# Kernel tuning notes

Measured on AMD Instinct MI355X. Metric: run time of the kernel, lower is better.

The kernel has to match this reference:

```python
import jax, jax.numpy as jnp
import numpy as np

N_NODES = 50000
N_EDGES = 800000
IN_FEAT = 64
HIDDEN = 128
NUM_LAYERS = 3


def setup_inputs() -> dict:
    key = jax.random.key(0)
    ks = jax.random.split(key, 8)
    x = jax.random.normal(ks[0], (N_NODES, IN_FEAT), dtype=jnp.float32)
    edge_index = jax.random.randint(ks[1], (2, N_EDGES), 0, N_NODES, dtype=jnp.int64)
    s_in = 1.0 / np.sqrt(IN_FEAT)
    s_h = 1.0 / np.sqrt(HIDDEN)
    W_in = jax.random.uniform(ks[2], (IN_FEAT, HIDDEN), jnp.float32, -s_in, s_in)
    b_in = jax.random.uniform(ks[3], (HIDDEN,), jnp.float32, -s_in, s_in)
    W_self = jax.random.uniform(ks[4], (NUM_LAYERS, HIDDEN, HIDDEN), jnp.float32, -s_h, s_h)
    b_self = jax.random.uniform(ks[5], (NUM_LAYERS, HIDDEN), jnp.float32, -s_h, s_h)
    W_nbr = jax.random.uniform(ks[6], (NUM_LAYERS, HIDDEN, HIDDEN), jnp.float32, -s_h, s_h)
    return {"x": x, "edge_index": edge_index, "W_in": W_in, "b_in": b_in,
            "W_self": W_self, "b_self": b_self, "W_nbr": W_nbr}


def reference(x, edge_index, W_in, b_in, W_self, b_self, W_nbr):
    # input projection: h [N, HIDDEN]
    h = x @ W_in + b_in
    src = edge_index[0]
    dst = edge_index[1]
    n = h.shape[0]
    ones = jnp.ones((dst.shape[0], 1), dtype=h.dtype)
    # scatter-mean denominator is grad-constant; compute once
    cnt = jax.ops.segment_sum(ones, dst, num_segments=n)
    cnt = jnp.maximum(cnt, 1.0)
    for l in range(W_self.shape[0]):
        msg = h[src] @ W_nbr[l]                               # [E, HIDDEN]
        agg = jax.ops.segment_sum(msg, dst, num_segments=n) / cnt  # scatter-mean
        h = jax.nn.elu(h @ W_self[l] + b_self[l] + agg)
    return h
```

## Files before the change

### kernel.cpp

```cpp
#include <hip/hip_runtime.h>
#include <cstdint>

#define HIDDEN 128

typedef unsigned short u16;
using frag_t   = __attribute__((ext_vector_type(8))) short;
using f32x4_t  = __attribute__((ext_vector_type(4))) float;
using ushort8_t = __attribute__((ext_vector_type(8))) unsigned short;

__device__ __forceinline__ float bf2f(u16 u) {
    union { unsigned int i; float f; } c;
    c.i = ((unsigned int)u) << 16;
    return c.f;
}
__device__ __forceinline__ u16 f2bf(float f) {
    unsigned int u = __float_as_uint(f);
    unsigned int r = (u + 0x7fffu + ((u >> 16) & 1u)) >> 16;
    return (u16)r;
}


__global__ void k_hist_prep(const int* __restrict__ ei, int E, int* __restrict__ deg, int npr,
                            const float* __restrict__ x,
                            const float* __restrict__ W_in,
                            const float* __restrict__ W_self,
                            const float* __restrict__ W_nbr,
                            u16* __restrict__ xf,
                            u16* __restrict__ WtI_hi, u16* __restrict__ WtI_lo,
                            u16* __restrict__ WtS_hi, u16* __restrict__ WtS_lo,
                            u16* __restrict__ WtN_hi, u16* __restrict__ WtN_lo,
                            int L, int nxg) {
    {
        int r  = blockIdx.x & 7;
        int lo = r * npr, hi = lo + npr;
        int nb = gridDim.x >> 3;
        int bi = blockIdx.x >> 3;
        int tid = bi * blockDim.x + threadIdx.x;
        int stride = nb * blockDim.x;
        if ((E & 3) == 0) {
            const int4* d4 = (const int4*)(ei + E);
            int nch = E >> 2;
            for (int c = tid; c < nch; c += stride) {
                int4 d = d4[c];
                if (d.x >= lo && d.x < hi) atomicAdd(&deg[d.x], 1);
                if (d.y >= lo && d.y < hi) atomicAdd(&deg[d.y], 1);
                if (d.z >= lo && d.z < hi) atomicAdd(&deg[d.z], 1);
                if (d.w >= lo && d.w < hi) atomicAdd(&deg[d.w], 1);
            }
        } else {
            for (int e = tid; e < E; e += stride) {
                int d = ei[E + e];
                if (d >= lo && d < hi) atomicAdd(&deg[d], 1);
            }
        }
    }
    {
        int nIn = 64 * 128;
        int nSq = L * 128 * 128;
        int wtot = nIn + 2 * nSq;
        int total = wtot + nxg;
        int stride = gridDim.x * blockDim.x;
        for (int i = blockIdx.x * blockDim.x + threadIdx.x; i < total; i += stride) {
            if (i >= wtot) {
                int t = i - wtot;
                int row = t >> 3, c = t & 7;
                const float4* xs = (const float4*)(x + (size_t)row * 64 + c * 8);
                float4 v0 = xs[0], v1 = xs[1];
                ushort8_t o;
                o[0] = f2bf(v0.x); o[1] = f2bf(v0.y); o[2] = f2bf(v0.z); o[3] = f2bf(v0.w);
                o[4] = f2bf(v1.x); o[5] = f2bf(v1.y); o[6] = f2bf(v1.z); o[7] = f2bf(v1.w);
                int T = row >> 4, m = row & 15;
                int f = c >> 2, q = c & 3;
                *(ushort8_t*)&xf[((size_t)(T * 2 + f) * 64 + q * 16 + m) * 8] = o;
            } else {
                float v; u16* phi; u16* plo; int o;
                if (i < nIn) {
                    int n = i / 64, k = i % 64;
                    v = W_in[k * 128 + n]; phi = WtI_hi; plo = WtI_lo; o = n * 64 + k;
                } else if (i < nIn + nSq) {
                    int t = i - nIn;
                    int l = t / (128 * 128), r = t % (128 * 128);
                    int n = r / 128, k = r % 128;
                    v = W_self[l * 128 * 128 + k * 128 + n]; phi = WtS_hi; plo = WtS_lo;
                    o = l * 128 * 128 + n * 128 + k;
                } else {
                    int t = i - nIn - nSq;
                    int l = t / (128 * 128), r = t % (128 * 128);
                    int n = r / 128, k = r % 128;
                    v = W_nbr[l * 128 * 128 + k * 128 + n]; phi = WtN_hi; plo = WtN_lo;
                    o = l * 128 * 128 + n * 128 + k;
                }
                u16 hi = f2bf(v);
                phi[o] = hi;
                plo[o] = f2bf(v - bf2f(hi));
            }
        }
    }
}

__global__ void k_scan1(const int* __restrict__ deg, int* __restrict__ rowp,
                        int* __restrict__ bsums, int n) {
    __shared__ int sh[1024];
    int t = threadIdx.x;
    int base = blockIdx.x * 1024;
    int v = (base + t < n) ? deg[base + t] : 0;
    sh[t] = v;
    __syncthreads();
    for (int off = 1; off < 1024; off <<= 1) {
        int x = sh[t];
        int y = (t >= off) ? sh[t - off] : 0;
        __syncthreads();
        sh[t] = x + y;
        __syncthreads();
    }
    if (base + t < n) rowp[base + t + 1] = sh[t];
    if (t == 1023) bsums[blockIdx.x] = sh[1023];
}

__global__ void k_scan_tail(int* __restrict__ rowp, const int* __restrict__ bsums,
                            int* __restrict__ fillp, int n, int nb) {
    __shared__ int sh[1024];
    int t = threadIdx.x;
    int b = blockIdx.x;
    sh[t] = (t < nb) ? bsums[t] : 0;
    __syncthreads();
    for (int off = 1; off < 1024; off <<= 1) {
        int x = sh[t];
        int y = (t >= off) ? sh[t - off] : 0;
        __syncthreads();
        sh[t] = x + y;
        __syncthreads();
    }
    int boff = (b == 0) ? 0 : sh[b - 1];
    int base = b * 1024;
    if (base + t < n) {
        int v = rowp[base + t + 1] + boff;
        rowp[base + t + 1] = v;
        if (base + t + 1 < n) fillp[base + t + 1] = v;
    }
    if (b == 0 && t == 0) { rowp[0] = 0; fillp[0] = 0; }
}


__device__ __forceinline__ void dev_fill(const int* __restrict__ ei, int E,
                                         int* __restrict__ fillpos, int* __restrict__ colx,
                                         int npr, int bid, int nbF) {
    int r  = bid & 7;
    int lo = r * npr, hi = lo + npr;
    int nb = nbF >> 3;
    int bi = bid >> 3;
    int tid = bi * blockDim.x + threadIdx.x;
    int stride = nb * blockDim.x;
    if ((E & 3) == 0) {
        const int4* s4 = (const int4*)ei;
        const int4* d4 = (const int4*)(ei + E);
        int nch = E >> 2;
        for (int c = tid; c < nch; c += stride) {
            int4 d = d4[c];
            bool m0 = d.x >= lo && d.x < hi;
            bool m1 = d.y >= lo && d.y < hi;
            bool m2 = d.z >= lo && d.z < hi;
            bool m3 = d.w >= lo && d.w < hi;
            if (m0 | m1 | m2 | m3) {
                int4 s = s4[c];
                if (m0) colx[atomicAdd(&fillpos[d.x], 1)] = s.x;
                if (m1) colx[atomicAdd(&fillpos[d.y], 1)] = s.y;
                if (m2) colx[atomicAdd(&fillpos[d.z], 1)] = s.z;
                if (m3) colx[atomicAdd(&fillpos[d.w], 1)] = s.w;
            }
        }
    } else {
        for (int e = tid; e < E; e += stride) {
            int d = ei[E + e];
            if (d >= lo && d < hi) colx[atomicAdd(&fillpos[d], 1)] = ei[e];
        }
    }
}


__global__ __launch_bounds__(256, 4) void k_agg(
        const ushort8_t* __restrict__ hb8, const int* __restrict__ rowp,
        const int* __restrict__ colx, u16* __restrict__ Sf, int n) {
    int g = (blockIdx.x * blockDim.x + threadIdx.x) >> 4;
    int lane = threadIdx.x & 15;
    if (g >= n) return;
    int beg = rowp[g];
    int end = rowp[g + 1];
    float a0[8], a1[8];
#pragma unroll
    for (int j = 0; j < 8; ++j) { a0[j] = 0.f; a1[j] = 0.f; }
    int e = beg;
    for (; e + 15 < end; e += 16) {
        int s0 = colx[e],      s1 = colx[e + 1],  s2 = colx[e + 2],  s3 = colx[e + 3];
        int s4 = colx[e + 4],  s5 = colx[e + 5],  s6 = colx[e + 6],  s7 = colx[e + 7];
        int s8 = colx[e + 8],  s9 = colx[e + 9],  sa = colx[e + 10], sb = colx[e + 11];
        int sc = colx[e + 12], sd = colx[e + 13], se = colx[e + 14], sf = colx[e + 15];
        ushort8_t v0 = hb8[(size_t)s0 * 16 + lane];
        ushort8_t v1 = hb8[(size_t)s1 * 16 + lane];
        ushort8_t v2 = hb8[(size_t)s2 * 16 + lane];
        ushort8_t v3 = hb8[(size_t)s3 * 16 + lane];
        ushort8_t v4 = hb8[(size_t)s4 * 16 + lane];
        ushort8_t v5 = hb8[(size_t)s5 * 16 + lane];
        ushort8_t v6 = hb8[(size_t)s6 * 16 + lane];
        ushort8_t v7 = hb8[(size_t)s7 * 16 + lane];
        ushort8_t v8 = hb8[(size_t)s8 * 16 + lane];
        ushort8_t v9 = hb8[(size_t)s9 * 16 + lane];
        ushort8_t va = hb8[(size_t)sa * 16 + lane];
        ushort8_t vb = hb8[(size_t)sb * 16 + lane];
        ushort8_t vc = hb8[(size_t)sc * 16 + lane];
        ushort8_t vd = hb8[(size_t)sd * 16 + lane];
        ushort8_t ve = hb8[(size_t)se * 16 + lane];
        ushort8_t vf = hb8[(size_t)sf * 16 + lane];
#pragma unroll
        for (int j = 0; j < 8; ++j) {
            a0[j] += bf2f(v0[j]); a1[j] += bf2f(v1[j]);
            a0[j] += bf2f(v2[j]); a1[j] += bf2f(v3[j]);
            a0[j] += bf2f(v4[j]); a1[j] += bf2f(v5[j]);
            a0[j] += bf2f(v6[j]); a1[j] += bf2f(v7[j]);
        }
#pragma unroll
        for (int j = 0; j < 8; ++j) {
            a0[j] += bf2f(v8[j]); a1[j] += bf2f(v9[j]);
            a0[j] += bf2f(va[j]); a1[j] += bf2f(vb[j]);
            a0[j] += bf2f(vc[j]); a1[j] += bf2f(vd[j]);
            a0[j] += bf2f(ve[j]); a1[j] += bf2f(vf[j]);
        }
    }
    for (; e + 7 < end; e += 8) {
        int s0 = colx[e],     s1 = colx[e + 1], s2 = colx[e + 2], s3 = colx[e + 3];
        int s4 = colx[e + 4], s5 = colx[e + 5], s6 = colx[e + 6], s7 = colx[e + 7];
        ushort8_t v0 = hb8[(size_t)s0 * 16 + lane];
        ushort8_t v1 = hb8[(size_t)s1 * 16 + lane];
        ushort8_t v2 = hb8[(size_t)s2 * 16 + lane];
        ushort8_t v3 = hb8[(size_t)s3 * 16 + lane];
        ushort8_t v4 = hb8[(size_t)s4 * 16 + lane];
        ushort8_t v5 = hb8[(size_t)s5 * 16 + lane];
        ushort8_t v6 = hb8[(size_t)s6 * 16 + lane];
        ushort8_t v7 = hb8[(size_t)s7 * 16 + lane];
#pragma unroll
        for (int j = 0; j < 8; ++j) {
            a0[j] += bf2f(v0[j]); a1[j] += bf2f(v1[j]);
            a0[j] += bf2f(v2[j]); a1[j] += bf2f(v3[j]);
            a0[j] += bf2f(v4[j]); a1[j] += bf2f(v5[j]);
            a0[j] += bf2f(v6[j]); a1[j] += bf2f(v7[j]);
        }
    }
    for (; e + 3 < end; e += 4) {
        int s0 = colx[e], s1 = colx[e + 1], s2 = colx[e + 2], s3 = colx[e + 3];
        ushort8_t v0 = hb8[(size_t)s0 * 16 + lane];
        ushort8_t v1 = hb8[(size_t)s1 * 16 + lane];
        ushort8_t v2 = hb8[(size_t)s2 * 16 + lane];
        ushort8_t v3 = hb8[(size_t)s3 * 16 + lane];
#pragma unroll
        for (int j = 0; j < 8; ++j) {
            a0[j] += bf2f(v0[j]); a1[j] += bf2f(v1[j]);
            a0[j] += bf2f(v2[j]); a1[j] += bf2f(v3[j]);
        }
    }
    for (; e < end; ++e) {
        int s = colx[e];
        ushort8_t v = hb8[(size_t)s * 16 + lane];
#pragma unroll
        for (int j = 0; j < 8; ++j) a0[j] += bf2f(v[j]);
    }
    int deg = end - beg;
    float inv = 1.0f / (float)(deg > 1 ? deg : 1);
    ushort8_t o;
#pragma unroll
    for (int j = 0; j < 8; ++j) o[j] = f2bf((a0[j] + a1[j]) * inv);
    int T = g >> 4, m = g & 15;
    *(ushort8_t*)&Sf[((size_t)(T * 4 + (lane >> 2)) * 64 + (lane & 3) * 16 + m) * 8] = o;
}


template <int KF1, int KF2, int DO_ELU>
__device__ __forceinline__ void dev_gemm(
    const u16* __restrict__ A1f, const u16* __restrict__ A2f,
    const u16* __restrict__ B1h, const u16* __restrict__ B1l,
    const u16* __restrict__ B2h, const u16* __restrict__ B2l,
    const float* __restrict__ bias, float* __restrict__ C,
    u16* __restrict__ Hrow, u16* __restrict__ Hf,
    int M, int bid, int gdim)
{
    constexpr int K1 = KF1 * 32;
    constexpr int K2 = KF2 * 32;
    constexpr int KF = KF1 + KF2;
    int lane = threadIdx.x & 63;
    int w    = threadIdx.x >> 6;
    int m16  = lane & 15;
    int quad = lane >> 4;
    int kq   = quad * 8;
    int ng   = (bid >> 3) & 1;
    int mtb  = (bid & 7) | ((bid >> 4) << 3);
    int ncol = (ng * 4 + w) * 16 + m16;

    frag_t bh[KF], bl[KF];
    if constexpr (KF1 > 0) {
#pragma unroll
        for (int f = 0; f < KF1; ++f) {
            bh[f] = *(const frag_t*)&B1h[(size_t)ncol * K1 + f * 32 + kq];
            bl[f] = *(const frag_t*)&B1l[(size_t)ncol * K1 + f * 32 + kq];
        }
    }
    if constexpr (KF2 > 0) {
#pragma unroll
        for (int f = 0; f < KF2; ++f) {
            bh[KF1 + f] = *(const frag_t*)&B2h[(size_t)ncol * K2 + f * 32 + kq];
            bl[KF1 + f] = *(const frag_t*)&B2l[(size_t)ncol * K2 + f * 32 + kq];
        }
    }

    float bv = bias[ncol];
    int nMT  = (M + 31) >> 5;
    int step = gdim >> 1;
    int fcol = ncol >> 5;
    int qcol = (ncol & 31) >> 3;
    int jcol = ncol & 7;

    auto loadA = [&](int mt, frag_t (&a0)[KF], frag_t (&a1)[KF]) {
        int T0 = mt * 2, T1 = T0 + 1;
        if constexpr (KF1 > 0) {
#pragma unroll
            for (int f = 0; f < KF1; ++f) {
                a0[f] = *(const frag_t*)&A1f[((size_t)(T0 * KF1 + f) * 64 + lane) * 8];
                a1[f] = *(const frag_t*)&A1f[((size_t)(T1 * KF1 + f) * 64 + lane) * 8];
            }
        }
        if constexpr (KF2 > 0) {
#pragma unroll
            for (int f = 0; f < KF2; ++f) {
                a0[KF1 + f] = *(const frag_t*)&A2f[((size_t)(T0 * KF2 + f) * 64 + lane) * 8];
                a1[KF1 + f] = *(const frag_t*)&A2f[((size_t)(T1 * KF2 + f) * 64 + lane) * 8];
            }
        }
    };

    auto compute = [&](int mt, frag_t (&a0)[KF], frag_t (&a1)[KF]) {
        f32x4_t acc0 = (f32x4_t){0.f, 0.f, 0.f, 0.f};
        f32x4_t acc1 = (f32x4_t){0.f, 0.f, 0.f, 0.f};
#pragma unroll
        for (int f = 0; f < KF; ++f) {
            acc0 = __builtin_amdgcn_mfma_f32_16x16x32_bf16(a0[f], bh[f], acc0, 0, 0, 0);
            acc1 = __builtin_amdgcn_mfma_f32_16x16x32_bf16(a1[f], bh[f], acc1, 0, 0, 0);
            acc0 = __builtin_amdgcn_mfma_f32_16x16x32_bf16(a0[f], bl[f], acc0, 0, 0, 0);
            acc1 = __builtin_amdgcn_mfma_f32_16x16x32_bf16(a1[f], bl[f], acc1, 0, 0, 0);
        }
        int rb = mt * 32 + quad * 4;
#pragma unroll
        for (int r = 0; r < 4; ++r) {
#pragma unroll
            for (int half = 0; half < 2; ++half) {
                int row = rb + r + half * 16;
                float av = half ? acc1[r] : acc0[r];
                if (row < M) {
                    float v = av + bv;
                    if constexpr (DO_ELU) v = (v > 0.f) ? v : expm1f(v);
                    if (C) C[(size_t)row * HIDDEN + ncol] = v;
                    if (Hrow) {
                        u16 hv = f2bf(v);
                        Hrow[(size_t)row * HIDDEN + ncol] = hv;
                        Hf[((size_t)((row >> 4) * 4 + fcol) * 64 + qcol * 16 + (row & 15)) * 8 + jcol] = hv;
                    }
                }
            }
        }
    };

    int mt = mtb;
    if (mt < nMT) {
        frag_t xa0[KF], xa1[KF], ya0[KF], ya1[KF];
        loadA(mt, xa0, xa1);
        while (true) {
            int mt2 = mt + step;
            if (mt2 < nMT) loadA(mt2, ya0, ya1);
            compute(mt, xa0, xa1);
            if (mt2 >= nMT) break;
            int mt3 = mt2 + step;
            if (mt3 < nMT) loadA(mt3, xa0, xa1);
            compute(mt2, ya0, ya1);
            if (mt3 >= nMT) break;
            mt = mt3;
        }
    }
}

template <int KF1, int KF2, int DO_ELU>
__global__ __launch_bounds__(256, 2) void k_gemm_mfma(
    const u16* __restrict__ A1f, const u16* __restrict__ A2f,
    const u16* __restrict__ B1h, const u16* __restrict__ B1l,
    const u16* __restrict__ B2h, const u16* __restrict__ B2l,
    const float* __restrict__ bias, float* __restrict__ C,
    u16* __restrict__ Hrow, u16* __restrict__ Hf, int M)
{
    dev_gemm<KF1, KF2, DO_ELU>(A1f, A2f, B1h, B1l, B2h, B2l, bias, C, Hrow, Hf,
                               M, blockIdx.x, gridDim.x);
}


__global__ __launch_bounds__(256, 2) void k_fill_gemm(
    const int* __restrict__ ei, int E, int* __restrict__ fillpos, int* __restrict__ colx,
    int npr, int nbF,
    const u16* __restrict__ xf,
    const u16* __restrict__ WtI_hi, const u16* __restrict__ WtI_lo,
    const float* __restrict__ b_in,
    u16* __restrict__ hRow, u16* __restrict__ hf, int M, int gdim)
{
    if (blockIdx.x < (unsigned)nbF) {
        dev_fill(ei, E, fillpos, colx, npr, blockIdx.x, nbF);
    } else {
        dev_gemm<2, 0, 0>(xf, nullptr, WtI_hi, WtI_lo, nullptr, nullptr,
                          b_in, nullptr, hRow, hf, M, blockIdx.x - nbF, gdim);
    }
}


extern "C" void kernel_launch(void* const* d_in, const int* in_sizes, int n_in,
                              void* d_out, int out_size, void* d_ws, size_t ws_size,
                              hipStream_t stream) {
    const float* x        = (const float*)d_in[0];
    const int* ei         = (const int*)d_in[1];
    const float* W_in     = (const float*)d_in[2];
    const float* b_in     = (const float*)d_in[3];
    const float* W_self   = (const float*)d_in[4];
    const float* b_self   = (const float*)d_in[5];
    const float* W_nbr    = (const float*)d_in[6];
    float* out = (float*)d_out;

    const int IN_FEAT = 64;
    int N = in_sizes[0] / IN_FEAT;
    int E = in_sizes[1] / 2;
    int L = in_sizes[4] / (HIDDEN * HIDDEN);

    char* ws = (char*)d_ws;
    size_t off = 0;
    auto alloc = [&](size_t bytes) -> void* {
        void* p = ws + off;
        off = (off + bytes + 255) & ~(size_t)255;
        return p;
    };

    int nT = ((N + 31) / 32) * 2;

    u16* hRowA = (u16*)alloc((size_t)N * HIDDEN * 2);
    u16* hRowB = (u16*)alloc((size_t)N * HIDDEN * 2);
    u16* hfA   = (u16*)alloc((size_t)nT * 4 * 64 * 8 * 2);
    u16* hfB   = (u16*)alloc((size_t)nT * 4 * 64 * 8 * 2);
    u16* xf    = (u16*)alloc((size_t)nT * 2 * 64 * 8 * 2);
    u16* Sf    = (u16*)alloc((size_t)nT * 4 * 64 * 8 * 2);
    u16* WtI_hi = (u16*)alloc(128 * 64 * 2);
    u16* WtI_lo = (u16*)alloc(128 * 64 * 2);
    u16* WtS_hi = (u16*)alloc((size_t)L * 128 * 128 * 2);
    u16* WtS_lo = (u16*)alloc((size_t)L * 128 * 128 * 2);
    u16* WtN_hi = (u16*)alloc((size_t)L * 128 * 128 * 2);
    u16* WtN_lo = (u16*)alloc((size_t)L * 128 * 128 * 2);
    int* deg   = (int*)alloc((size_t)N * sizeof(int));
    int* rowp  = (int*)alloc((size_t)(N + 1) * sizeof(int));
    int* fillp = (int*)alloc((size_t)N * sizeof(int));
    int* colx  = (int*)alloc((size_t)E * sizeof(int));
    int* bsums = (int*)alloc(1024 * sizeof(int));

    int npr = (N + 7) / 8;

    hipMemsetAsync(deg, 0, (size_t)N * sizeof(int), stream);
    int wtot = 64 * 128 + 2 * L * 128 * 128;
    (void)wtot;
    k_hist_prep<<<2048, 256, 0, stream>>>(ei, E, deg, npr,
                                          x, W_in, W_self, W_nbr, xf,
                                          WtI_hi, WtI_lo, WtS_hi, WtS_lo,
                                          WtN_hi, WtN_lo, L, N * 8);
    int nb = (N + 1023) / 1024;
    k_scan1<<<nb, 1024, 0, stream>>>(deg, rowp, bsums, N);
    k_scan_tail<<<nb, 1024, 0, stream>>>(rowp, bsums, fillp, N, nb);

    const int GB = 1024;
    const int NBF = 2048;

    k_fill_gemm<<<NBF + GB, 256, 0, stream>>>(
        ei, E, fillp, colx, npr, NBF,
        xf, WtI_hi, WtI_lo, b_in, hRowA, hfA, N, GB);

    u16* curRow = hRowA; u16* curF = hfA;
    u16* nxtRow = hRowB; u16* nxtF = hfB;

    for (int l = 0; l < L; ++l) {
        k_agg<<<(N + 15) / 16, 256, 0, stream>>>((const ushort8_t*)curRow, rowp, colx, Sf, N);
        const u16* Wsh = WtS_hi + (size_t)l * 128 * 128;
        const u16* Wsl = WtS_lo + (size_t)l * 128 * 128;
        const u16* Wnh = WtN_hi + (size_t)l * 128 * 128;
        const u16* Wnl = WtN_lo + (size_t)l * 128 * 128;
        const float* bs = b_self + (size_t)l * HIDDEN;
        bool last = (l == L - 1);
        k_gemm_mfma<4, 4, 1><<<GB, 256, 0, stream>>>(
            curF, Sf,
            Wsh, Wsl, Wnh, Wnl,
            bs, last ? out : nullptr,
            last ? nullptr : nxtRow, last ? nullptr : nxtF, N);
        u16* tr = curRow; curRow = nxtRow; nxtRow = tr;
        u16* tf = curF;   curF = nxtF;     nxtF = tf;
    }
}
```

Baseline: 326.7 us.

## Build CSR with per-chunk LDS histograms instead of global atomics

```diff
diff --git a/kernel.cpp b/kernel.cpp
--- a/kernel.cpp
+++ b/kernel.cpp
@@ -2,6 +2,9 @@
 #include <cstdint>
 
 #define HIDDEN 128
+#define NC 32
+#define NR 8
+#define MAXNPR 6400
 
 typedef unsigned short u16;
 using frag_t   = __attribute__((ext_vector_type(8))) short;
@@ -20,40 +23,48 @@
 }
 
 
-__global__ void k_hist_prep(const int* __restrict__ ei, int E, int* __restrict__ deg, int npr,
-                            const float* __restrict__ x,
-                            const float* __restrict__ W_in,
-                            const float* __restrict__ W_self,
-                            const float* __restrict__ W_nbr,
-                            u16* __restrict__ xf,
-                            u16* __restrict__ WtI_hi, u16* __restrict__ WtI_lo,
-                            u16* __restrict__ WtS_hi, u16* __restrict__ WtS_lo,
-                            u16* __restrict__ WtN_hi, u16* __restrict__ WtN_lo,
-                            int L, int nxg) {
-    {
-        int r  = blockIdx.x & 7;
-        int lo = r * npr, hi = lo + npr;
-        int nb = gridDim.x >> 3;
-        int bi = blockIdx.x >> 3;
-        int tid = bi * blockDim.x + threadIdx.x;
-        int stride = nb * blockDim.x;
-        if ((E & 3) == 0) {
-            const int4* d4 = (const int4*)(ei + E);
-            int nch = E >> 2;
-            for (int c = tid; c < nch; c += stride) {
-                int4 d = d4[c];
-                if (d.x >= lo && d.x < hi) atomicAdd(&deg[d.x], 1);
-                if (d.y >= lo && d.y < hi) atomicAdd(&deg[d.y], 1);
-                if (d.z >= lo && d.z < hi) atomicAdd(&deg[d.z], 1);
-                if (d.w >= lo && d.w < hi) atomicAdd(&deg[d.w], 1);
-            }
-        } else {
-            for (int e = tid; e < E; e += stride) {
-                int d = ei[E + e];
-                if (d >= lo && d < hi) atomicAdd(&deg[d], 1);
-            }
-        }
-    }
+__global__ __launch_bounds__(256) void k_hist2_prep(
+    const int* __restrict__ ei, int E, int* __restrict__ counts, int npr, int n,
+    const float* __restrict__ x,
+    const float* __restrict__ W_in,
+    const float* __restrict__ W_self,
+    const float* __restrict__ W_nbr,
+    u16* __restrict__ xf,
+    u16* __restrict__ WtI_hi, u16* __restrict__ WtI_lo,
+    u16* __restrict__ WtS_hi, u16* __restrict__ WtS_lo,
+    u16* __restrict__ WtN_hi, u16* __restrict__ WtN_lo,
+    int L, int nxg)
+{
+    __shared__ int lh[MAXNPR];
+    int r = blockIdx.x & (NR - 1);
+    int j = blockIdx.x >> 3;
+    int lo = r * npr;
+    int hi = lo + npr; if (hi > n) hi = n;
+    int nr = hi - lo;
+    for (int i = threadIdx.x; i < nr; i += 256) lh[i] = 0;
+    __syncthreads();
+
+    int nch4 = E >> 2;
+    int c0 = (int)((long long)j * nch4 / NC);
+    int c1 = (int)((long long)(j + 1) * nch4 / NC);
+    const int4* d4 = (const int4*)(ei + E);
+    for (int c = c0 + threadIdx.x; c < c1; c += 256) {
+        int4 d = d4[c];
+        if (d.x >= lo && d.x < hi) atomicAdd(&lh[d.x - lo], 1);
+        if (d.y >= lo && d.y < hi) atomicAdd(&lh[d.y - lo], 1);
+        if (d.z >= lo && d.z < hi) atomicAdd(&lh[d.z - lo], 1);
+        if (d.w >= lo && d.w < hi) atomicAdd(&lh[d.w - lo], 1);
+    }
+    if (j == NC - 1 && (E & 3)) {
+        for (int e = (nch4 << 2) + threadIdx.x; e < E; e += 256) {
+            int d = ei[E + e];
+            if (d >= lo && d < hi) atomicAdd(&lh[d - lo], 1);
+        }
+    }
+    __syncthreads();
+    for (int i = threadIdx.x; i < nr; i += 256)
+        counts[(size_t)j * n + lo + i] = lh[i];
+
     {
         int nIn = 64 * 128;
         int nSq = L * 128 * 128;
@@ -75,104 +86,124 @@
             } else {
                 float v; u16* phi; u16* plo; int o;
                 if (i < nIn) {
-                    int n = i / 64, k = i % 64;
-                    v = W_in[k * 128 + n]; phi = WtI_hi; plo = WtI_lo; o = n * 64 + k;
+                    int nn = i / 64, k = i % 64;
+                    v = W_in[k * 128 + nn]; phi = WtI_hi; plo = WtI_lo; o = nn * 64 + k;
                 } else if (i < nIn + nSq) {
                     int t = i - nIn;
-                    int l = t / (128 * 128), r = t % (128 * 128);
-                    int n = r / 128, k = r % 128;
-                    v = W_self[l * 128 * 128 + k * 128 + n]; phi = WtS_hi; plo = WtS_lo;
-                    o = l * 128 * 128 + n * 128 + k;
+                    int l = t / (128 * 128), rr = t % (128 * 128);
+                    int nn = rr / 128, k = rr % 128;
+                    v = W_self[l * 128 * 128 + k * 128 + nn]; phi = WtS_hi; plo = WtS_lo;
+                    o = l * 128 * 128 + nn * 128 + k;
                 } else {
                     int t = i - nIn - nSq;
-                    int l = t / (128 * 128), r = t % (128 * 128);
-                    int n = r / 128, k = r % 128;
-                    v = W_nbr[l * 128 * 128 + k * 128 + n]; phi = WtN_hi; plo = WtN_lo;
-                    o = l * 128 * 128 + n * 128 + k;
+                    int l = t / (128 * 128), rr = t % (128 * 128);
+                    int nn = rr / 128, k = rr % 128;
+                    v = W_nbr[l * 128 * 128 + k * 128 + nn]; phi = WtN_hi; plo = WtN_lo;
+                    o = l * 128 * 128 + nn * 128 + k;
                 }
-                u16 hi = f2bf(v);
-                phi[o] = hi;
-                plo[o] = f2bf(v - bf2f(hi));
+                u16 hiv = f2bf(v);
+                phi[o] = hiv;
+                plo[o] = f2bf(v - bf2f(hiv));
             }
         }
     }
+}
+
+
+__global__ void k_deg(const int* __restrict__ counts, int* __restrict__ deg,
+                      int* __restrict__ base, int n) {
+    int v = blockIdx.x * blockDim.x + threadIdx.x;
+    if (v >= n) return;
+    int run = 0;
+#pragma unroll
+    for (int j = 0; j < NC; ++j) {
+        int c = counts[(size_t)j * n + v];
+        base[(size_t)j * n + v] = run;
+        run += c;
+    }
+    deg[v] = run;
 }
 
 __global__ void k_scan1(const int* __restrict__ deg, int* __restrict__ rowp,
                         int* __restrict__ bsums, int n) {
     __shared__ int sh[1024];
     int t = threadIdx.x;
-    int base = blockIdx.x * 1024;
-    int v = (base + t < n) ? deg[base + t] : 0;
+    int bb = blockIdx.x * 1024;
+    int v = (bb + t < n) ? deg[bb + t] : 0;
     sh[t] = v;
     __syncthreads();
     for (int off = 1; off < 1024; off <<= 1) {
-        int x = sh[t];
+        int xx = sh[t];
         int y = (t >= off) ? sh[t - off] : 0;
         __syncthreads();
-        sh[t] = x + y;
+        sh[t] = xx + y;
         __syncthreads();
     }
-    if (base + t < n) rowp[base + t + 1] = sh[t];
+    if (bb + t < n) rowp[bb + t + 1] = sh[t];
     if (t == 1023) bsums[blockIdx.x] = sh[1023];
 }
 
 __global__ void k_scan_tail(int* __restrict__ rowp, const int* __restrict__ bsums,
-                            int* __restrict__ fillp, int n, int nb) {
+                            int n, int nb) {
     __shared__ int sh[1024];
     int t = threadIdx.x;
     int b = blockIdx.x;
     sh[t] = (t < nb) ? bsums[t] : 0;
     __syncthreads();
     for (int off = 1; off < 1024; off <<= 1) {
-        int x = sh[t];
+        int xx = sh[t];
         int y = (t >= off) ? sh[t - off] : 0;
         __syncthreads();
-        sh[t] = x + y;
+        sh[t] = xx + y;
         __syncthreads();
     }
     int boff = (b == 0) ? 0 : sh[b - 1];
-    int base = b * 1024;
-    if (base + t < n) {
-        int v = rowp[base + t + 1] + boff;
-        rowp[base + t + 1] = v;
-        if (base + t + 1 < n) fillp[base + t + 1] = v;
-    }
-    if (b == 0 && t == 0) { rowp[0] = 0; fillp[0] = 0; }
-}
-
-
-__device__ __forceinline__ void dev_fill(const int* __restrict__ ei, int E,
-                                         int* __restrict__ fillpos, int* __restrict__ colx,
-                                         int npr, int bid, int nbF) {
-    int r  = bid & 7;
-    int lo = r * npr, hi = lo + npr;
-    int nb = nbF >> 3;
-    int bi = bid >> 3;
-    int tid = bi * blockDim.x + threadIdx.x;
-    int stride = nb * blockDim.x;
-    if ((E & 3) == 0) {
-        const int4* s4 = (const int4*)ei;
-        const int4* d4 = (const int4*)(ei + E);
-        int nch = E >> 2;
-        for (int c = tid; c < nch; c += stride) {
-            int4 d = d4[c];
-            bool m0 = d.x >= lo && d.x < hi;
-            bool m1 = d.y >= lo && d.y < hi;
-            bool m2 = d.z >= lo && d.z < hi;
-            bool m3 = d.w >= lo && d.w < hi;
-            if (m0 | m1 | m2 | m3) {
-                int4 s = s4[c];
-                if (m0) colx[atomicAdd(&fillpos[d.x], 1)] = s.x;
-                if (m1) colx[atomicAdd(&fillpos[d.y], 1)] = s.y;
-                if (m2) colx[atomicAdd(&fillpos[d.z], 1)] = s.z;
-                if (m3) colx[atomicAdd(&fillpos[d.w], 1)] = s.w;
+    int bb = b * 1024;
+    if (bb + t < n) rowp[bb + t + 1] += boff;
+    if (b == 0 && t == 0) rowp[0] = 0;
+}
+
+
+__device__ __forceinline__ void dev_fill2(const int* __restrict__ ei, int E,
+                                          const int* __restrict__ rowp,
+                                          const int* __restrict__ base,
+                                          int* __restrict__ colx,
+                                          int npr, int n, int bid, int* lh) {
+    int r = bid & (NR - 1);
+    int j = bid >> 3;
+    int lo = r * npr;
+    int hi = lo + npr; if (hi > n) hi = n;
+    int nr = hi - lo;
+    for (int i = threadIdx.x; i < nr; i += 256) lh[i] = 0;
+    __syncthreads();
+
+    int nch4 = E >> 2;
+    int c0 = (int)((long long)j * nch4 / NC);
+    int c1 = (int)((long long)(j + 1) * nch4 / NC);
+    const int4* s4 = (const int4*)ei;
+    const int4* d4 = (const int4*)(ei + E);
+    const int* basej = base + (size_t)j * n;
+    for (int c = c0 + threadIdx.x; c < c1; c += 256) {
+        int4 d = d4[c];
+        bool m0 = d.x >= lo && d.x < hi;
+        bool m1 = d.y >= lo && d.y < hi;
+        bool m2 = d.z >= lo && d.z < hi;
+        bool m3 = d.w >= lo && d.w < hi;
+        if (m0 | m1 | m2 | m3) {
+            int4 s = s4[c];
+            if (m0) { int sl = atomicAdd(&lh[d.x - lo], 1); colx[rowp[d.x] + basej[d.x] + sl] = s.x; }
+            if (m1) { int sl = atomicAdd(&lh[d.y - lo], 1); colx[rowp[d.y] + basej[d.y] + sl] = s.y; }
+            if (m2) { int sl = atomicAdd(&lh[d.z - lo], 1); colx[rowp[d.z] + basej[d.z] + sl] = s.z; }
+            if (m3) { int sl = atomicAdd(&lh[d.w - lo], 1); colx[rowp[d.w] + basej[d.w] + sl] = s.w; }
+        }
+    }
+    if (j == NC - 1 && (E & 3)) {
+        for (int e = (nch4 << 2) + threadIdx.x; e < E; e += 256) {
+            int d = ei[E + e];
+            if (d >= lo && d < hi) {
+                int sl = atomicAdd(&lh[d - lo], 1);
+                colx[rowp[d] + basej[d] + sl] = ei[e];
             }
-        }
-    } else {
-        for (int e = tid; e < E; e += stride) {
-            int d = ei[E + e];
-            if (d >= lo && d < hi) colx[atomicAdd(&fillpos[d], 1)] = ei[e];
         }
     }
 }
@@ -397,16 +428,18 @@
 }
 
 
-__global__ __launch_bounds__(256, 2) void k_fill_gemm(
-    const int* __restrict__ ei, int E, int* __restrict__ fillpos, int* __restrict__ colx,
-    int npr, int nbF,
+__global__ __launch_bounds__(256, 2) void k_fill2_gemm(
+    const int* __restrict__ ei, int E,
+    const int* __restrict__ rowp, const int* __restrict__ base,
+    int* __restrict__ colx, int npr, int n, int nbF,
     const u16* __restrict__ xf,
     const u16* __restrict__ WtI_hi, const u16* __restrict__ WtI_lo,
     const float* __restrict__ b_in,
     u16* __restrict__ hRow, u16* __restrict__ hf, int M, int gdim)
 {
+    __shared__ int cur[MAXNPR];
     if (blockIdx.x < (unsigned)nbF) {
-        dev_fill(ei, E, fillpos, colx, npr, blockIdx.x, nbF);
+        dev_fill2(ei, E, rowp, base, colx, npr, n, blockIdx.x, cur);
     } else {
         dev_gemm<2, 0, 0>(xf, nullptr, WtI_hi, WtI_lo, nullptr, nullptr,
                           b_in, nullptr, hRow, hf, M, blockIdx.x - nbF, gdim);
@@ -453,30 +486,29 @@
     u16* WtS_lo = (u16*)alloc((size_t)L * 128 * 128 * 2);
     u16* WtN_hi = (u16*)alloc((size_t)L * 128 * 128 * 2);
     u16* WtN_lo = (u16*)alloc((size_t)L * 128 * 128 * 2);
+    int* counts = (int*)alloc((size_t)NC * N * sizeof(int));
+    int* base   = (int*)alloc((size_t)NC * N * sizeof(int));
     int* deg   = (int*)alloc((size_t)N * sizeof(int));
     int* rowp  = (int*)alloc((size_t)(N + 1) * sizeof(int));
-    int* fillp = (int*)alloc((size_t)N * sizeof(int));
     int* colx  = (int*)alloc((size_t)E * sizeof(int));
     int* bsums = (int*)alloc(1024 * sizeof(int));
 
-    int npr = (N + 7) / 8;
-
-    hipMemsetAsync(deg, 0, (size_t)N * sizeof(int), stream);
-    int wtot = 64 * 128 + 2 * L * 128 * 128;
-    (void)wtot;
-    k_hist_prep<<<2048, 256, 0, stream>>>(ei, E, deg, npr,
-                                          x, W_in, W_self, W_nbr, xf,
-                                          WtI_hi, WtI_lo, WtS_hi, WtS_lo,
-                                          WtN_hi, WtN_lo, L, N * 8);
+    int npr = (N + NR - 1) / NR;
+
+    k_hist2_prep<<<NR * NC, 256, 0, stream>>>(ei, E, counts, npr, N,
+                                              x, W_in, W_self, W_nbr, xf,
+                                              WtI_hi, WtI_lo, WtS_hi, WtS_lo,
+                                              WtN_hi, WtN_lo, L, N * 8);
+    k_deg<<<(N + 255) / 256, 256, 0, stream>>>(counts, deg, base, N);
     int nb = (N + 1023) / 1024;
     k_scan1<<<nb, 1024, 0, stream>>>(deg, rowp, bsums, N);
-    k_scan_tail<<<nb, 1024, 0, stream>>>(rowp, bsums, fillp, N, nb);
+    k_scan_tail<<<nb, 1024, 0, stream>>>(rowp, bsums, N, nb);
 
     const int GB = 1024;
-    const int NBF = 2048;
-
-    k_fill_gemm<<<NBF + GB, 256, 0, stream>>>(
-        ei, E, fillp, colx, npr, NBF,
+    const int NBF = NR * NC;
+
+    k_fill2_gemm<<<NBF + GB, 256, 0, stream>>>(
+        ei, E, rowp, base, colx, npr, N, NBF,
         xf, WtI_hi, WtI_lo, b_in, hRowA, hfA, N, GB);
 
     u16* curRow = hRowA; u16* curF = hfA;
```

Measured after the change: 310.3 us. 1.05x faster.
